# Performance work log

Measured on AMD Instinct MI355X. Metric: run time of the kernel, lower is better.

The kernel has to match this reference:

```python
import jax, jax.numpy as jnp
import numpy as np

B = 256
H = W = 14
HW = H * W
TS = 0.03  # sigmoid temperature
TC = 0.07  # contrastive temperature
TP_K = int(HW * 0.1)   # 19
TN_K = int(HW * 0.5)   # 98
EPS_NORM = 1e-12
EPS_PD = 1e-6  # torch F.pairwise_distance eps


def _l2norm(x, axis):
    n = jnp.sqrt(jnp.sum(x * x, axis=axis, keepdims=True))
    return x / jnp.maximum(n, EPS_NORM)


def _conv(x, w):
    return jax.lax.conv_general_dilated(
        x, w, window_strides=(1, 1), padding='SAME',
        dimension_numbers=('NCHW', 'OIHW', 'NCHW'))


def setup_inputs() -> dict:
    key = jax.random.key(0)
    ks = jax.random.split(key, 7)
    ev = jax.random.normal(ks[0], (B, 384, H, W), dtype=jnp.float32)
    ea = jax.random.normal(ks[1], (B, 2048), dtype=jnp.float32)
    masks = jax.random.randint(ks[2], (B, H, W), 0, 2).astype(jnp.int32)
    masks = masks.at[:, 0, 0].set(1)  # guarantee nonzero mask area
    W_fc1 = jax.random.normal(ks[3], (512, 2048), dtype=jnp.float32) * 0.02
    W_fc2 = jax.random.normal(ks[4], (512, 512), dtype=jnp.float32) * 0.02
    W_conv1 = jax.random.normal(ks[5], (512, 384, 3, 3), dtype=jnp.float32) * 0.02
    W_conv2 = jax.random.normal(ks[6], (512, 512, 3, 3), dtype=jnp.float32) * 0.02
    return {'ev': ev, 'ea': ea, 'masks': masks, 'W_fc1': W_fc1,
            'W_fc2': W_fc2, 'W_conv1': W_conv1, 'W_conv2': W_conv2}


def reference(ev, ea, masks, W_fc1, W_fc2, W_conv1, W_conv2):
    # Audio_Proj: fc2(relu(fc1(ea)))  -> (B, 512)
    fa = jnp.maximum(ea @ W_fc1.T, 0.0) @ W_fc2.T

    # Visual_Proj: conv2(relu(conv1(ev))) -> (B, 512, 14, 14)
    fv_map = _conv(jnp.maximum(_conv(ev, W_conv1), 0.0), W_conv2)
    fv_map_norm = _l2norm(fv_map, axis=1)

    # masked mean pooling over the Ncut mask -> indicator vector (B, 512)
    m = masks.astype(jnp.float32)
    ind_vec = jnp.sum(fv_map * m[:, None], axis=(2, 3)) / jnp.sum(m, axis=(1, 2))[:, None]
    ind_vec_norm = _l2norm(ind_vec, axis=1)

    # Sij[i, j, p] = <fv_map_norm[i, :, p], ind_vec_norm[j]>  -> (B, B, HW)
    Sij = jnp.einsum('ichw,jc->ijhw', fv_map_norm, ind_vec_norm).reshape(B, B, HW)

    # per-row topk thresholds (kth largest / kth smallest)
    pos_thr = jax.lax.top_k(Sij, TP_K)[0][..., -1:]           # (B, B, 1)
    neg_thr = -jax.lax.top_k(-Sij, TN_K)[0][..., -1:]         # (B, B, 1)

    m_p = jax.nn.sigmoid((Sij - pos_thr) / TS)
    m_n = 1.0 - jax.nn.sigmoid((Sij - neg_thr) / TS)

    SP = jnp.sum(Sij * m_p, axis=-1) / jnp.sum(m_p, axis=-1)  # (B, B)
    SN = jnp.sum(Sij * m_n, axis=-1) / jnp.sum(m_n, axis=-1)  # (B, B)

    logits1 = jnp.concatenate([SP, SN], axis=1) / TC          # (B, 2B)
    logits2 = jnp.concatenate([SP.T, SN.T], axis=1) / TC
    labels = jnp.arange(B)
    loss1 = -jnp.mean(jax.nn.log_softmax(logits1, axis=-1)[labels, labels])
    loss2 = -jnp.mean(jax.nn.log_softmax(logits2, axis=-1)[labels, labels])

    # squared pairwise distance between detached ind_vec and fa (torch eps in diff)
    diff = jax.lax.stop_gradient(ind_vec)[:, None, :] - fa[None, :, :] + EPS_PD
    dist_mat = jnp.sum(diff * diff, axis=-1)                  # (B, B)

    ivn_d = jax.lax.stop_gradient(ind_vec_norm)
    vv_logits = ivn_d @ ivn_d.T
    eye = jnp.eye(B, dtype=jnp.float32)
    w = -vv_logits * (1.0 - eye) + eye
    dist_mat = dist_mat * w

    mask_mat = eye - (1.0 - eye) / (B - 1)
    loss3 = jnp.mean(jnp.maximum(jnp.sum(dist_mat * mask_mat, axis=1) + 0.6, 0.0))
    loss4 = jnp.mean(jnp.maximum(jnp.sum(dist_mat * mask_mat, axis=0) + 0.6, 0.0))

    return ((loss1 + loss2) / 2.0, (loss3 + loss4) / 2.0)
```

## Files before the change

### kernel.cpp

```cpp
#include <hip/hip_runtime.h>
#include <stdint.h>


typedef __attribute__((ext_vector_type(8))) short bf16x8;
typedef __attribute__((ext_vector_type(4))) float f32x4;

__device__ __forceinline__ unsigned short f2bf(float x) {
  unsigned u = __float_as_uint(x);
  unsigned r = u + 0x7FFFu + ((u >> 16) & 1u);
  return (unsigned short)(r >> 16);
}
__device__ __forceinline__ float bf2f(unsigned short h) {
  return __uint_as_float(((unsigned)h) << 16);
}

typedef const __attribute__((address_space(1))) void* gptr1_t;
typedef __attribute__((address_space(3))) void* lptr3_t;
__device__ __forceinline__ void gload_lds16(const void* g, void* l) {
  __builtin_amdgcn_global_load_lds((gptr1_t)g, (lptr3_t)l, 16, 0, 0);
}

__device__ __forceinline__ float waveSum(float v) {
#pragma unroll
  for (int m = 1; m < 64; m <<= 1) v += __shfl_xor(v, m, 64);
  return v;
}
__device__ __forceinline__ float waveMax(float v) {
#pragma unroll
  for (int m = 1; m < 64; m <<= 1) v = fmaxf(v, __shfl_xor(v, m, 64));
  return v;
}
template <int NW>
__device__ __forceinline__ float blockSum(float v) {
  __shared__ float sh[NW];
  v = waveSum(v);
  int wv = threadIdx.x >> 6, ln = threadIdx.x & 63;
  if (ln == 0) sh[wv] = v;
  __syncthreads();
  float r = 0.f;
#pragma unroll
  for (int w = 0; w < NW; ++w) r += sh[w];
  __syncthreads();
  return r;
}
template <int NW>
__device__ __forceinline__ float blockMax(float v) {
  __shared__ float sh[NW];
  v = waveMax(v);
  int wv = threadIdx.x >> 6, ln = threadIdx.x & 63;
  if (ln == 0) sh[wv] = v;
  __syncthreads();
  float r = -3.4e38f;
#pragma unroll
  for (int w = 0; w < NW; ++w) r = fmaxf(r, sh[w]);
  __syncthreads();
  return r;
}

#define RA 65536

template <int KC, int EPI>
__global__ __launch_bounds__(256, 2) void convtap6_k(
    const unsigned short* __restrict__ A, const unsigned short* __restrict__ Bw,
    unsigned short* __restrict__ C) {
  __shared__ __align__(16) short Ah[256 * 72];
  __shared__ __align__(16) short Bb[2][128 * 72];
  const int tid = threadIdx.x;
  const int wave = tid >> 6, lane = tid & 63;
  const int wm = wave >> 1, wn = wave & 1;
  const int quad = lane >> 4, tq = lane & 15;
  const int img = blockIdx.x, n0 = blockIdx.y * 128;

  int pab[7];
  {
    const int dh = tq >> 3;
    int wq = wm * 8 + (tq & 7);
    if (wq == 0) wq = 8;
    else if (wq == 15) wq = 7;
#pragma unroll
    for (int mi = 0; mi < 7; ++mi) {
      int pr = (1 + 2 * mi + dh) * 16 + wq;
      pab[mi] = pr * 72 + quad * 8;
    }
  }
  int nb[4];
#pragma unroll
  for (int ni = 0; ni < 4; ++ni)
    nb[ni] = (wn * 64 + ni * 16 + tq) * 72 + quad * 8;

  const char* Ab = (const char*)A;
  const char* Bg = (const char*)Bw;
  const int l16 = lane * 16;

  f32x4 acc[7][4];
#pragma unroll
  for (int mi = 0; mi < 7; ++mi)
#pragma unroll
    for (int ni = 0; ni < 4; ++ni) {
      f32x4 z = {0.f, 0.f, 0.f, 0.f};
      acc[mi][ni] = z;
    }

  auto stageA = [&](int kc) {
    size_t s0 = ((size_t)kc * RA + img * 256) * 144;
#pragma unroll
    for (int i = 0; i < 9; ++i) {
      int c = wave + i * 4;
      gload_lds16(Ab + s0 + (size_t)c * 1024 + l16, (char*)Ah + c * 1024);
    }
  };
  auto stageB = [&](int t, int kc, int buf) {
    size_t s0 = ((size_t)(t * KC + kc) * 512 + n0) * 144;
#pragma unroll
    for (int i = 0; i < 5; ++i) {
      int c = wave + i * 4;
      if (c < 18)
        gload_lds16(Bg + s0 + (size_t)c * 1024 + l16, (char*)Bb[buf] + c * 1024);
    }
  };

  stageA(0);
  stageB(0, 0, 0);
  __syncthreads();

  const int NS = KC * 9;
#pragma unroll 1
  for (int s = 0; s < NS; ++s) {
    int kc = s / 9, t = s - kc * 9;
    if (s + 1 < NS) {
      int kc1 = (s + 1) / 9, t1 = (s + 1) - kc1 * 9;
      stageB(t1, kc1, (s + 1) & 1);
    }
    const int aoff = (((t / 3) - 1) * 16 + (t % 3) - 1) * 72;
    const short* Bc = Bb[s & 1];
#pragma unroll
    for (int h = 0; h < 2; ++h) {
      bf16x8 af[7], bf[4];
#pragma unroll
      for (int mi = 0; mi < 7; ++mi)
        af[mi] = *(const bf16x8*)&Ah[pab[mi] + aoff + h * 32];
#pragma unroll
      for (int ni = 0; ni < 4; ++ni)
        bf[ni] = *(const bf16x8*)&Bc[nb[ni] + h * 32];
#pragma unroll
      for (int mi = 0; mi < 7; ++mi)
#pragma unroll
        for (int ni = 0; ni < 4; ++ni)
          acc[mi][ni] = __builtin_amdgcn_mfma_f32_16x16x32_bf16(
              af[mi], bf[ni], acc[mi][ni], 0, 0, 0);
    }
    __syncthreads();
    if (t == 8 && kc + 1 < KC) {
      stageA(kc + 1);
      __syncthreads();
    }
  }

#pragma unroll
  for (int mi = 0; mi < 7; ++mi) {
#pragma unroll
    for (int r = 0; r < 4; ++r) {
      int idx = quad * 4 + r;
      int wv = wm * 8 + (idx & 7);
      if (wv == 0 || wv == 15) continue;
      int hh = 1 + 2 * mi + (idx >> 3);
      if (EPI == 0) {
        int cell = img * 256 + hh * 16 + wv;
        int slice = (n0 >> 6) + wn;
        size_t ob = ((size_t)slice * RA + cell) * 72 + tq;
#pragma unroll
        for (int ni = 0; ni < 4; ++ni)
          C[ob + ni * 16] = f2bf(fmaxf(acc[mi][ni][r], 0.f));
      } else {
        int p = (hh - 1) * 14 + (wv - 1);
        size_t ob = (size_t)(img * 196 + p) * 512 + n0 + wn * 64 + tq;
#pragma unroll
        for (int ni = 0; ni < 4; ++ni)
          C[ob + ni * 16] = f2bf(acc[mi][ni][r]);
      }
    }
  }
}

template <int K, int NLD, int EPI>
__global__ __launch_bounds__(256, 2) void gemm1_k(
    const unsigned short* __restrict__ A, const unsigned short* __restrict__ Bw,
    void* __restrict__ C, const float* __restrict__ rs) {
  __shared__ short As[128 * 64];
  __shared__ short Bs[128 * 64];
  const int tid = threadIdx.x;
  const int wave = tid >> 6, lane = tid & 63;
  const int m0 = blockIdx.x * 128, n0 = blockIdx.y * 128;
  const int rr8 = lane >> 3, seg = lane & 7, gseg = seg ^ rr8;
  const int wm = wave >> 1, wn = wave & 1;
  const int quad = lane >> 4, tq = lane & 15;

  size_t asrc[4], bsrc[4];
#pragma unroll
  for (int i8 = 0; i8 < 4; ++i8) {
    int rloc = wave * 32 + i8 * 8 + rr8;
    asrc[i8] = (size_t)(m0 + rloc) * K + gseg * 8;
    bsrc[i8] = (size_t)(n0 + rloc) * K + gseg * 8;
  }

  f32x4 acc[4][4];
#pragma unroll
  for (int mi = 0; mi < 4; ++mi)
#pragma unroll
    for (int ni = 0; ni < 4; ++ni) {
      f32x4 z = {0.f, 0.f, 0.f, 0.f};
      acc[mi][ni] = z;
    }

#pragma unroll 1
  for (int kc2 = 0; kc2 < K / 64; ++kc2) {
    int kb = kc2 * 64;
    __syncthreads();
#pragma unroll
    for (int i8 = 0; i8 < 4; ++i8) {
      gload_lds16(A + asrc[i8] + kb, &As[(wave * 32 + i8 * 8) * 64]);
      gload_lds16(Bw + bsrc[i8] + kb, &Bs[(wave * 32 + i8 * 8) * 64]);
    }
    __syncthreads();
#pragma unroll
    for (int h = 0; h < 2; ++h) {
      bf16x8 af[4], bfr[4];
#pragma unroll
      for (int mi = 0; mi < 4; ++mi) {
        int row = wm * 64 + mi * 16 + tq;
        af[mi] = *(const bf16x8*)&As[row * 64 +
                                     ((((h << 2) | quad) ^ (row & 7)) << 3)];
      }
#pragma unroll
      for (int ni = 0; ni < 4; ++ni) {
        int row = wn * 64 + ni * 16 + tq;
        bfr[ni] = *(const bf16x8*)&Bs[row * 64 +
                                      ((((h << 2) | quad) ^ (row & 7)) << 3)];
      }
#pragma unroll
      for (int mi = 0; mi < 4; ++mi)
#pragma unroll
        for (int ni = 0; ni < 4; ++ni)
          acc[mi][ni] = __builtin_amdgcn_mfma_f32_16x16x32_bf16(
              af[mi], bfr[ni], acc[mi][ni], 0, 0, 0);
    }
  }

#pragma unroll
  for (int mi = 0; mi < 4; ++mi) {
#pragma unroll
    for (int r = 0; r < 4; ++r) {
      int m = m0 + wm * 64 + mi * 16 + quad * 4 + r;
      float sc = (EPI == 3) ? rs[m] : 1.f;
      size_t obase = (size_t)m * NLD + n0 + wn * 64 + tq;
#pragma unroll
      for (int ni = 0; ni < 4; ++ni) {
        float v = acc[mi][ni][r];
        size_t idx = obase + ni * 16;
        if (EPI == 0)
          ((unsigned short*)C)[idx] = f2bf(fmaxf(v, 0.f));
        else if (EPI == 2)
          ((float*)C)[idx] = v;
        else
          ((float*)C)[idx] = v * sc;
      }
    }
  }
}

__global__ __launch_bounds__(256, 2) void gemm_xv_k(
    const unsigned short* __restrict__ ivpb, const unsigned short* __restrict__ fab,
    const unsigned short* __restrict__ indnb, float* __restrict__ Xm,
    float* __restrict__ Vm) {
  const unsigned short* A = blockIdx.z ? indnb : ivpb;
  const unsigned short* Bw = blockIdx.z ? indnb : fab;
  float* C = blockIdx.z ? Vm : Xm;
  __shared__ short As[128 * 64];
  __shared__ short Bs[128 * 64];
  const int tid = threadIdx.x;
  const int wave = tid >> 6, lane = tid & 63;
  const int m0 = blockIdx.x * 128, n0 = blockIdx.y * 128;
  const int rr8 = lane >> 3, seg = lane & 7, gseg = seg ^ rr8;
  const int wm = wave >> 1, wn = wave & 1;
  const int quad = lane >> 4, tq = lane & 15;
  size_t asrc[4], bsrc[4];
#pragma unroll
  for (int i8 = 0; i8 < 4; ++i8) {
    int rloc = wave * 32 + i8 * 8 + rr8;
    asrc[i8] = (size_t)(m0 + rloc) * 512 + gseg * 8;
    bsrc[i8] = (size_t)(n0 + rloc) * 512 + gseg * 8;
  }
  f32x4 acc[4][4];
#pragma unroll
  for (int mi = 0; mi < 4; ++mi)
#pragma unroll
    for (int ni = 0; ni < 4; ++ni) {
      f32x4 z = {0.f, 0.f, 0.f, 0.f};
      acc[mi][ni] = z;
    }
#pragma unroll 1
  for (int kc2 = 0; kc2 < 8; ++kc2) {
    int kb = kc2 * 64;
    __syncthreads();
#pragma unroll
    for (int i8 = 0; i8 < 4; ++i8) {
      gload_lds16(A + asrc[i8] + kb, &As[(wave * 32 + i8 * 8) * 64]);
      gload_lds16(Bw + bsrc[i8] + kb, &Bs[(wave * 32 + i8 * 8) * 64]);
    }
    __syncthreads();
#pragma unroll
    for (int h = 0; h < 2; ++h) {
      bf16x8 af[4], bfr[4];
#pragma unroll
      for (int mi = 0; mi < 4; ++mi) {
        int row = wm * 64 + mi * 16 + tq;
        af[mi] = *(const bf16x8*)&As[row * 64 +
                                     ((((h << 2) | quad) ^ (row & 7)) << 3)];
      }
#pragma unroll
      for (int ni = 0; ni < 4; ++ni) {
        int row = wn * 64 + ni * 16 + tq;
        bfr[ni] = *(const bf16x8*)&Bs[row * 64 +
                                      ((((h << 2) | quad) ^ (row & 7)) << 3)];
      }
#pragma unroll
      for (int mi = 0; mi < 4; ++mi)
#pragma unroll
        for (int ni = 0; ni < 4; ++ni)
          acc[mi][ni] = __builtin_amdgcn_mfma_f32_16x16x32_bf16(
              af[mi], bfr[ni], acc[mi][ni], 0, 0, 0);
    }
  }
#pragma unroll
  for (int mi = 0; mi < 4; ++mi)
#pragma unroll
    for (int r = 0; r < 4; ++r) {
      int m = m0 + wm * 64 + mi * 16 + quad * 4 + r;
      size_t obase = (size_t)m * 256 + n0 + wn * 64 + tq;
#pragma unroll
      for (int ni = 0; ni < 4; ++ni) C[obase + ni * 16] = acc[mi][ni][r];
    }
}

__global__ void prep_all_k(const float* __restrict__ ea,
                           const float* __restrict__ Wf1,
                           const float* __restrict__ Wf2,
                           const float* __restrict__ Wc1,
                           const float* __restrict__ Wc2,
                           unsigned short* __restrict__ eab,
                           unsigned short* __restrict__ wf1b,
                           unsigned short* __restrict__ wf2b,
                           unsigned short* __restrict__ wb1,
                           unsigned short* __restrict__ wb2,
                           unsigned int* __restrict__ x1u) {
  int i = blockIdx.x * 256 + threadIdx.x;
  if (i < 524288) {
    eab[i] = f2bf(ea[i]);
  } else if (i < 1572864) {
    int j = i - 524288;
    wf1b[j] = f2bf(Wf1[j]);
  } else if (i < 1835008) {
    int j = i - 1572864;
    wf2b[j] = f2bf(Wf2[j]);
  } else if (i < 3604480) {
    int j = i - 1835008;
    int t = j / (6 * 512 * 64), r = j - t * (6 * 512 * 64);
    int kc = r / (512 * 64), r2 = r - kc * (512 * 64);
    int n = r2 >> 6, c = r2 & 63;
    wb1[((size_t)(t * 6 + kc) * 512 + n) * 72 + c] =
        f2bf(Wc1[(n * 384 + kc * 64 + c) * 9 + t]);
  } else if (i < 5963776) {
    int j = i - 3604480;
    int t = j / (8 * 512 * 64), r = j - t * (8 * 512 * 64);
    int kc = r / (512 * 64), r2 = r - kc * (512 * 64);
    int n = r2 >> 6, c = r2 & 63;
    wb2[((size_t)(t * 8 + kc) * 512 + n) * 72 + c] =
        f2bf(Wc2[(n * 512 + kc * 64 + c) * 9 + t]);
  } else {
    int j = i - 5963776;
    int hr = j >> 8, u = j & 255;
    int slice = u >> 5, uu = u & 31;
    int b = hr / 60, c = hr - b * 60;
    int cell;
    if (c < 16) cell = c;
    else if (c < 32) cell = 240 + (c - 16);
    else if (c < 46) cell = (c - 31) * 16;
    else cell = (c - 45) * 16 + 15;
    x1u[((size_t)slice * RA + b * 256 + cell) * 36 + uu] = 0u;
  }
}

__global__ __launch_bounds__(256) void evpad_k(const float* __restrict__ ev,
                                               unsigned short* __restrict__ out) {
  int b = blockIdx.x, ct = blockIdx.y;
  __shared__ float tile[64][197];
  int tid = threadIdx.x;
  const float* src = ev + ((size_t)b * 384 + ct * 64) * 196;
#pragma unroll 1
  for (int it = 0; it < 49; ++it) {
    int idx = it * 256 + tid;
    int c = idx / 196, p = idx - c * 196;
    tile[c][p] = src[idx];
  }
  __syncthreads();
  unsigned short* dst = out + ((size_t)ct * RA + b * 256) * 72;
#pragma unroll 1
  for (int it = 0; it < 64; ++it) {
    int idx = it * 256 + tid;
    int cell = idx >> 6, c = idx & 63;
    int h = (cell >> 4) - 1, w = (cell & 15) - 1;
    float v = ((unsigned)h < 14u && (unsigned)w < 14u) ? tile[c][h * 14 + w]
                                                       : 0.f;
    dst[(size_t)cell * 72 + c] = f2bf(v);
  }
}


__global__ __launch_bounds__(512) void pool_k(
    const unsigned short* __restrict__ fv, const int* __restrict__ masks,
    unsigned short* __restrict__ indnb, unsigned short* __restrict__ ivpb,
    float* __restrict__ Pi, float* __restrict__ rn) {
  int b = blockIdx.x;
  int w = threadIdx.x >> 6, lane = threadIdx.x & 63;
  __shared__ float red[8][512];
  __shared__ float msh[8];
  float acc[8] = {0.f, 0.f, 0.f, 0.f, 0.f, 0.f, 0.f, 0.f};
  float msum = 0.f;
  for (int p = w; p < 196; p += 8) {
    float m = (float)masks[b * 196 + p];
    msum += m;
    uint4 d = *(const uint4*)(fv + (size_t)(b * 196 + p) * 512 + lane * 8);
    const unsigned short* hp = (const unsigned short*)&d;
    float ss = 0.f;
#pragma unroll
    for (int k = 0; k < 8; ++k) {
      float x = bf2f(hp[k]);
      ss += x * x;
      acc[k] += m * x;
    }
    ss = waveSum(ss);
    if (lane == 0) rn[b * 196 + p] = 1.f / fmaxf(sqrtf(ss), 1e-12f);
  }
#pragma unroll
  for (int k = 0; k < 8; ++k) red[w][lane * 8 + k] = acc[k];
  if (lane == 0) msh[w] = msum;
  __syncthreads();
  int tid = threadIdx.x;
  float s = 0.f, mtot = 0.f;
#pragma unroll
  for (int ww = 0; ww < 8; ++ww) {
    s += red[ww][tid];
    mtot += msh[ww];
  }
  float v = s / mtot;
  float ss2 = blockSum<8>(v * v);
  float sc = 1.f / fmaxf(sqrtf(ss2), 1e-12f);
  indnb[b * 512 + tid] = f2bf(v * sc);
  float ve = v + 1e-6f;
  ivpb[b * 512 + tid] = f2bf(ve);
  float p2 = blockSum<8>(ve * ve);
  if (tid == 0) Pi[b] = p2;
}

__global__ __launch_bounds__(512) void fanorm_k(const float* __restrict__ fa,
                                                unsigned short* __restrict__ fab,
                                                float* __restrict__ Qj) {
  int b = blockIdx.x, tid = threadIdx.x;
  float v = fa[b * 512 + tid];
  fab[b * 512 + tid] = f2bf(v);
  float q = blockSum<8>(v * v);
  if (tid == 0) Qj[b] = q;
}


__device__ __forceinline__ float radix_kth(unsigned k0, unsigned k1, unsigned k2,
                                           unsigned k3, int k) {
  unsigned prefix = 0;
  int kk = k;
#pragma unroll 1
  for (int bit = 31; bit >= 14; --bit) {
    unsigned thi = (prefix >> bit) | 1u;
    int c = __popcll(__ballot((k0 >> bit) == thi)) +
            __popcll(__ballot((k1 >> bit) == thi)) +
            __popcll(__ballot((k2 >> bit) == thi)) +
            __popcll(__ballot((k3 >> bit) == thi));
    if (kk <= c)
      prefix |= (1u << bit);
    else
      kk -= c;
  }
  unsigned u = (prefix & 0x80000000u) ? (prefix ^ 0x80000000u) : ~prefix;
  return __uint_as_float(u);
}
__device__ __forceinline__ unsigned sortkey(float x) {
  unsigned u = __float_as_uint(x);
  return u ^ (((int)u >> 31) | 0x80000000u);
}

__global__ __launch_bounds__(256) void spsn_k(const float* __restrict__ Sij,
                                              float* __restrict__ SP,
                                              float* __restrict__ SN) {
  int i = blockIdx.x, jg = blockIdx.y;
  int tid = threadIdx.x, wave = tid >> 6, lane = tid & 63;
  __shared__ float tile[196 * 65];
#pragma unroll 1
  for (int it = 0; it < 49; ++it) {
    int lin = it * 256 + tid;
    int p = lin >> 6, j = lin & 63;
    tile[p * 65 + j] = Sij[(size_t)(i * 196 + p) * 256 + jg * 64 + j];
  }
  __syncthreads();
#pragma unroll 1
  for (int jj = 0; jj < 16; ++jj) {
    int j = jj * 4 + wave;
    float v0 = tile[lane * 65 + j];
    float v1 = tile[(lane + 64) * 65 + j];
    float v2 = tile[(lane + 128) * 65 + j];
    bool val3 = lane < 4;
    float v3 = val3 ? tile[(lane + 192) * 65 + j] : 0.f;
    unsigned k0 = sortkey(v0), k1 = sortkey(v1), k2 = sortkey(v2);
    unsigned k3 = val3 ? sortkey(v3) : 0u;
    float thrP = radix_kth(k0, k1, k2, k3, 19);
    float thrN = radix_kth(k0, k1, k2, k3, 99);
    float spn = 0.f, spd = 0.f, snn = 0.f, snd = 0.f;
    const float invTS = 1.f / 0.03f;
#pragma unroll
    for (int q = 0; q < 4; ++q) {
      float v = (q == 0) ? v0 : (q == 1) ? v1 : (q == 2) ? v2 : v3;
      bool ok = (q < 3) || val3;
      if (ok) {
        float mp = 1.f / (1.f + __expf((thrP - v) * invTS));
        float mn = 1.f / (1.f + __expf((v - thrN) * invTS));
        spn += v * mp;
        spd += mp;
        snn += v * mn;
        snd += mn;
      }
    }
    spn = waveSum(spn); spd = waveSum(spd);
    snn = waveSum(snn); snd = waveSum(snd);
    if (lane == 0) {
      SP[i * 256 + jg * 64 + j] = spn / spd;
      SN[i * 256 + jg * 64 + j] = snn / snd;
    }
  }
}

__global__ __launch_bounds__(256) void loss12_k(const float* __restrict__ SP,
                                                const float* __restrict__ SN,
                                                float* __restrict__ out) {
  int r = blockIdx.x;
  int i = r & 255;
  bool col = r >= 256;
  int tid = threadIdx.x;
  const float invTC = 1.f / 0.07f;
  float a = (col ? SP[tid * 256 + i] : SP[i * 256 + tid]) * invTC;
  float b = (col ? SN[tid * 256 + i] : SN[i * 256 + tid]) * invTC;
  float mx = blockMax<4>(fmaxf(a, b));
  float se = blockSum<4>(__expf(a - mx) + __expf(b - mx));
  float lse = mx + __logf(se);
  if (tid == 0) {
    float diag = SP[i * 256 + i] * invTC;
    atomicAdd(out, -(diag - lse) * (1.f / 512.f));
  }
}

__global__ __launch_bounds__(256) void distcomb_k(
    const float* __restrict__ Pi, const float* __restrict__ Qj,
    const float* __restrict__ X, const float* __restrict__ V,
    float* __restrict__ val, float* __restrict__ out) {
  int i = blockIdx.x, j = threadIdx.x;
  float d = Pi[i] - 2.f * X[i * 256 + j] + Qj[j];
  float w = (i == j) ? 1.f : -V[i * 256 + j];
  float x = d * w;
  val[i * 256 + j] = x;
  __shared__ float diag_sh;
  if (j == i) diag_sh = x;
  float tot = blockSum<4>(x);
  if (j == 0) {
    float rs = diag_sh - (tot - diag_sh) * (1.f / 255.f);
    atomicAdd(out + 1, fmaxf(rs + 0.6f, 0.f) * (1.f / 512.f));
  }
}

__global__ __launch_bounds__(256) void loss4_k(const float* __restrict__ val,
                                               float* __restrict__ out) {
  int j = blockIdx.x, i = threadIdx.x;
  float x = val[i * 256 + j];
  __shared__ float diag_sh;
  if (i == j) diag_sh = x;
  float tot = blockSum<4>(x);
  if (i == 0) {
    float cs = diag_sh - (tot - diag_sh) * (1.f / 255.f);
    atomicAdd(out + 1, fmaxf(cs + 0.6f, 0.f) * (1.f / 512.f));
  }
}


extern "C" void kernel_launch(void* const* d_in, const int* in_sizes, int n_in,
                              void* d_out, int out_size, void* d_ws,
                              size_t ws_size, hipStream_t stream) {
  (void)in_sizes; (void)n_in; (void)out_size; (void)ws_size;
  const float* ev = (const float*)d_in[0];
  const float* ea = (const float*)d_in[1];
  const int* msk = (const int*)d_in[2];
  const float* Wf1 = (const float*)d_in[3];
  const float* Wf2 = (const float*)d_in[4];
  const float* Wc1 = (const float*)d_in[5];
  const float* Wc2 = (const float*)d_in[6];
  float* out = (float*)d_out;
  char* ws = (char*)d_ws;

  size_t off = 0;
  auto alloc = [&](size_t bytes) {
    void* p = ws + off;
    off = (off + bytes + 255) & ~(size_t)255;
    return p;
  };
  unsigned short* evb = (unsigned short*)alloc((size_t)6 * RA * 144);
  unsigned short* fv = evb;
  unsigned short* x1b = (unsigned short*)alloc((size_t)8 * RA * 144);
  float* Sij = (float*)x1b;
  unsigned short* wb1 = (unsigned short*)alloc((size_t)9 * 6 * 512 * 144);
  unsigned short* wb2 = (unsigned short*)alloc((size_t)9 * 8 * 512 * 144);
  unsigned short* eab = (unsigned short*)alloc((size_t)256 * 2048 * 2);
  unsigned short* wf1b = (unsigned short*)alloc((size_t)512 * 2048 * 2);
  unsigned short* wf2b = (unsigned short*)alloc((size_t)512 * 512 * 2);
  unsigned short* hb = (unsigned short*)alloc((size_t)256 * 512 * 2);
  float* fa = (float*)alloc((size_t)256 * 512 * 4);
  unsigned short* indnb = (unsigned short*)alloc((size_t)256 * 512 * 2);
  unsigned short* ivpb = (unsigned short*)alloc((size_t)256 * 512 * 2);
  unsigned short* fab = (unsigned short*)alloc((size_t)256 * 512 * 2);
  float* Pi = (float*)alloc(256 * 4);
  float* Qj = (float*)alloc(256 * 4);
  float* Xm = (float*)alloc((size_t)256 * 256 * 4);
  float* Vm = (float*)alloc((size_t)256 * 256 * 4);
  float* rn = (float*)alloc((size_t)50176 * 4);
  float* SP = (float*)alloc((size_t)256 * 256 * 4);
  float* SN = (float*)alloc((size_t)256 * 256 * 4);
  float* val = (float*)alloc((size_t)256 * 256 * 4);

  hipMemsetAsync(out, 0, 2 * sizeof(float), stream);

  prep_all_k<<<38656, 256, 0, stream>>>(ea, Wf1, Wf2, Wc1, Wc2, eab, wf1b,
                                        wf2b, wb1, wb2, (unsigned int*)x1b);
  evpad_k<<<dim3(256, 6), 256, 0, stream>>>(ev, evb);

  convtap6_k<6, 0><<<dim3(256, 4), 256, 0, stream>>>(evb, wb1, x1b);
  gemm1_k<2048, 512, 0><<<dim3(2, 4), 256, 0, stream>>>(eab, wf1b, hb, nullptr);
  gemm1_k<512, 512, 2><<<dim3(2, 4), 256, 0, stream>>>(hb, wf2b, fa, nullptr);
  convtap6_k<8, 1><<<dim3(256, 4), 256, 0, stream>>>(x1b, wb2, fv);

  pool_k<<<256, 512, 0, stream>>>(fv, msk, indnb, ivpb, Pi, rn);
  fanorm_k<<<256, 512, 0, stream>>>(fa, fab, Qj);

  gemm1_k<512, 256, 3><<<dim3(392, 2), 256, 0, stream>>>(fv, indnb, Sij, rn);
  gemm_xv_k<<<dim3(2, 2, 2), 256, 0, stream>>>(ivpb, fab, indnb, Xm, Vm);

  spsn_k<<<dim3(256, 4), 256, 0, stream>>>(Sij, SP, SN);
  loss12_k<<<512, 256, 0, stream>>>(SP, SN, out);
  distcomb_k<<<256, 256, 0, stream>>>(Pi, Qj, Xm, Vm, val, out);
  loss4_k<<<256, 256, 0, stream>>>(val, out);
}
```

Baseline: 803.5 us.

## Load conv weight fragments directly from global memory in MFMA-ready layout

Measured after the change: 840.3 us. 4.6% more time.

```diff
diff --git a/kernel.cpp b/kernel.cpp
--- a/kernel.cpp
+++ b/kernel.cpp
@@ -64,7 +64,6 @@
     const unsigned short* __restrict__ A, const unsigned short* __restrict__ Bw,
     unsigned short* __restrict__ C) {
   __shared__ __align__(16) short Ah[256 * 72];
-  __shared__ __align__(16) short Bb[2][128 * 72];
   const int tid = threadIdx.x;
   const int wave = tid >> 6, lane = tid & 63;
   const int wm = wave >> 1, wn = wave & 1;
@@ -83,13 +82,9 @@
       pab[mi] = pr * 72 + quad * 8;
     }
   }
-  int nb[4];
-#pragma unroll
-  for (int ni = 0; ni < 4; ++ni)
-    nb[ni] = (wn * 64 + ni * 16 + tq) * 72 + quad * 8;
+  const int gb = (n0 >> 4) + wn * 4;
 
   const char* Ab = (const char*)A;
-  const char* Bg = (const char*)Bw;
   const int l16 = lane * 16;
 
   f32x4 acc[7][4];
@@ -109,48 +104,46 @@
       gload_lds16(Ab + s0 + (size_t)c * 1024 + l16, (char*)Ah + c * 1024);
     }
   };
-  auto stageB = [&](int t, int kc, int buf) {
-    size_t s0 = ((size_t)(t * KC + kc) * 512 + n0) * 144;
-#pragma unroll
-    for (int i = 0; i < 5; ++i) {
-      int c = wave + i * 4;
-      if (c < 18)
-        gload_lds16(Bg + s0 + (size_t)c * 1024 + l16, (char*)Bb[buf] + c * 1024);
-    }
-  };
 
   stageA(0);
-  stageB(0, 0, 0);
   __syncthreads();
 
   const int NS = KC * 9;
 #pragma unroll 1
   for (int s = 0; s < NS; ++s) {
     int kc = s / 9, t = s - kc * 9;
-    if (s + 1 < NS) {
-      int kc1 = (s + 1) / 9, t1 = (s + 1) - kc1 * 9;
-      stageB(t1, kc1, (s + 1) & 1);
-    }
+    const int b16 = (t * KC + kc) * 4096 + gb * 128 + lane;
+    bf16x8 bw0[4];
+#pragma unroll
+    for (int ni = 0; ni < 4; ++ni)
+      bw0[ni] = *(const bf16x8*)&Bw[(size_t)(b16 + ni * 128) * 8];
     const int aoff = (((t / 3) - 1) * 16 + (t % 3) - 1) * 72;
-    const short* Bc = Bb[s & 1];
-#pragma unroll
-    for (int h = 0; h < 2; ++h) {
-      bf16x8 af[7], bf[4];
-#pragma unroll
-      for (int mi = 0; mi < 7; ++mi)
-        af[mi] = *(const bf16x8*)&Ah[pab[mi] + aoff + h * 32];
+    bf16x8 af0[7];
+#pragma unroll
+    for (int mi = 0; mi < 7; ++mi)
+      af0[mi] = *(const bf16x8*)&Ah[pab[mi] + aoff];
+    bf16x8 bw1[4];
+#pragma unroll
+    for (int ni = 0; ni < 4; ++ni)
+      bw1[ni] = *(const bf16x8*)&Bw[(size_t)(b16 + ni * 128 + 64) * 8];
+#pragma unroll
+    for (int mi = 0; mi < 7; ++mi)
 #pragma unroll
       for (int ni = 0; ni < 4; ++ni)
-        bf[ni] = *(const bf16x8*)&Bc[nb[ni] + h * 32];
-#pragma unroll
-      for (int mi = 0; mi < 7; ++mi)
-#pragma unroll
-        for (int ni = 0; ni < 4; ++ni)
-          acc[mi][ni] = __builtin_amdgcn_mfma_f32_16x16x32_bf16(
-              af[mi], bf[ni], acc[mi][ni], 0, 0, 0);
-    }
-    __syncthreads();
+        acc[mi][ni] = __builtin_amdgcn_mfma_f32_16x16x32_bf16(
+            af0[mi], bw0[ni], acc[mi][ni], 0, 0, 0);
+    bf16x8 af1[7];
+#pragma unroll
+    for (int mi = 0; mi < 7; ++mi)
+      af1[mi] = *(const bf16x8*)&Ah[pab[mi] + aoff + 32];
+#pragma unroll
+    for (int mi = 0; mi < 7; ++mi)
+#pragma unroll
+      for (int ni = 0; ni < 4; ++ni)
+        acc[mi][ni] = __builtin_amdgcn_mfma_f32_16x16x32_bf16(
+            af1[mi], bw1[ni], acc[mi][ni], 0, 0, 0);
     if (t == 8 && kc + 1 < KC) {
+      __syncthreads();
       stageA(kc + 1);
       __syncthreads();
     }
@@ -364,18 +357,20 @@
     wf2b[j] = f2bf(Wf2[j]);
   } else if (i < 3604480) {
     int j = i - 1835008;
-    int t = j / (6 * 512 * 64), r = j - t * (6 * 512 * 64);
-    int kc = r / (512 * 64), r2 = r - kc * (512 * 64);
-    int n = r2 >> 6, c = r2 & 63;
-    wb1[((size_t)(t * 6 + kc) * 512 + n) * 72 + c] =
-        f2bf(Wc1[(n * 384 + kc * 64 + c) * 9 + t]);
+    int t = j / (6 * 32768), r = j - t * (6 * 32768);
+    int kc = r / 32768, r2 = r - kc * 32768;
+    int g = r2 >> 10, h = (r2 >> 9) & 1, quad = (r2 >> 7) & 3;
+    int tq = (r2 >> 3) & 15, jj = r2 & 7;
+    int n = g * 16 + tq, cin = kc * 64 + h * 32 + quad * 8 + jj;
+    wb1[j] = f2bf(Wc1[(n * 384 + cin) * 9 + t]);
   } else if (i < 5963776) {
     int j = i - 3604480;
-    int t = j / (8 * 512 * 64), r = j - t * (8 * 512 * 64);
-    int kc = r / (512 * 64), r2 = r - kc * (512 * 64);
-    int n = r2 >> 6, c = r2 & 63;
-    wb2[((size_t)(t * 8 + kc) * 512 + n) * 72 + c] =
-        f2bf(Wc2[(n * 512 + kc * 64 + c) * 9 + t]);
+    int t = j / (8 * 32768), r = j - t * (8 * 32768);
+    int kc = r / 32768, r2 = r - kc * 32768;
+    int g = r2 >> 10, h = (r2 >> 9) & 1, quad = (r2 >> 7) & 3;
+    int tq = (r2 >> 3) & 15, jj = r2 & 7;
+    int n = g * 16 + tq, cin = kc * 64 + h * 32 + quad * 8 + jj;
+    wb2[j] = f2bf(Wc2[(n * 512 + cin) * 9 + t]);
   } else {
     int j = i - 5963776;
     int hr = j >> 8, u = j & 255;
@@ -621,8 +616,8 @@
   unsigned short* fv = evb;
   unsigned short* x1b = (unsigned short*)alloc((size_t)8 * RA * 144);
   float* Sij = (float*)x1b;
-  unsigned short* wb1 = (unsigned short*)alloc((size_t)9 * 6 * 512 * 144);
-  unsigned short* wb2 = (unsigned short*)alloc((size_t)9 * 8 * 512 * 144);
+  unsigned short* wb1 = (unsigned short*)alloc((size_t)9 * 6 * 32768 * 2);
+  unsigned short* wb2 = (unsigned short*)alloc((size_t)9 * 8 * 32768 * 2);
   unsigned short* eab = (unsigned short*)alloc((size_t)256 * 2048 * 2);
   unsigned short* wf1b = (unsigned short*)alloc((size_t)512 * 2048 * 2);
   unsigned short* wf2b = (unsigned short*)alloc((size_t)512 * 512 * 2);
```
